# Performance work log

Hardware: AMD Instinct MI355X
Metric: run time of the kernel (lower is better)

The kernel has to match this reference:

```python
import jax, jax.numpy as jnp
import numpy as np

DIM = 64      # d_model, expand=1 -> d_inner = DIM
H_IN = 128
W_IN = 128
DS = 8        # d_state
DTR = 4       # dt_rank = ceil(DIM/16)
DCONV = 4     # conv kernel size
NDIR = 4      # bimamba v6: h-fwd, h-bwd, w-fwd, w-bwd


def layernorm(x, g, b, eps=1e-5):
    m = x.mean(-1, keepdims=True)
    v = x.var(-1, keepdims=True)
    return (x - m) / jnp.sqrt(v + eps) * g + b


def causal_conv(x, w, b):
    # x: (B, L, D), w: (D, 1, K) depthwise, causal left pad
    xt = x.transpose(0, 2, 1)  # (B, D, L)
    y = jax.lax.conv_general_dilated(xt, w, (1,), [(DCONV - 1, 0)],
                                     feature_group_count=xt.shape[1])
    return y.transpose(0, 2, 1) + b


def selective_scan(u, delta, A, Bm, Cm, D):
    # u,delta: (B,L,D); A: (D,N); Bm,Cm: (B,L,N); D: (D,)
    dA = jnp.exp(delta[..., None] * A)                       # (B,L,D,N)
    dBu = delta[..., None] * Bm[:, :, None, :] * u[..., None]

    def comb(c1, c2):
        a1, b1 = c1
        a2, b2 = c2
        return a1 * a2, a2 * b1 + b2

    _, hs = jax.lax.associative_scan(comb, (dA, dBu), axis=1)  # (B,L,D,N)
    return jnp.einsum('bldn,bln->bld', hs, Cm) + u * D


def setup_inputs() -> dict:
    key = jax.random.key(0)
    ks = jax.random.split(key, 12)
    s = 0.02
    inp = {
        'input': jax.random.normal(ks[0], (2, DIM, H_IN, W_IN), jnp.float32),
        'ln_g': jnp.ones((DIM,), jnp.float32),
        'ln_b': jnp.zeros((DIM,), jnp.float32),
        'in_proj_w': jax.random.normal(ks[1], (2 * DIM, DIM), jnp.float32) * s,
        'conv_w': jax.random.normal(ks[2], (NDIR, DIM, 1, DCONV), jnp.float32) * s,
        'conv_b': jnp.zeros((NDIR, DIM), jnp.float32),
        'xproj_w': jax.random.normal(ks[3], (NDIR, DTR + 2 * DS, DIM), jnp.float32) * s,
        'dtproj_w': jax.random.normal(ks[4], (NDIR, DIM, DTR), jnp.float32) * s,
        'dtproj_b': jax.random.normal(ks[5], (NDIR, DIM), jnp.float32) * 0.1,
        'A_log': jnp.broadcast_to(jnp.log(jnp.arange(1.0, DS + 1.0, dtype=jnp.float32)),
                                  (NDIR, DIM, DS)).copy(),
        'D_skip': jnp.ones((NDIR, DIM), jnp.float32),
        'on_g': jnp.ones((DIM,), jnp.float32),
        'on_b': jnp.zeros((DIM,), jnp.float32),
        'out_proj_w': jax.random.normal(ks[6], (DIM, DIM), jnp.float32) * s,
    }
    return inp


def reference(input, ln_g, ln_b, in_proj_w, conv_w, conv_b, xproj_w,
              dtproj_w, dtproj_b, A_log, D_skip, on_g, on_b, out_proj_w):
    B, C, H, W = input.shape
    L = H * W
    seq = input.reshape(B, C, L).transpose(0, 2, 1)           # b (h w) c
    seq = layernorm(seq, ln_g, ln_b)
    xz = seq @ in_proj_w.T                                    # (B,L,2D)
    x, z = jnp.split(xz, 2, axis=-1)

    ar = jnp.arange(L)
    perm = (ar % H) * W + ar // H    # (h w) -> (w h)
    inv = (ar % W) * H + ar // W     # (w h) -> (h w)

    dirs = [(None, False), (None, True), (perm, False), (perm, True)]
    y_sum = jnp.zeros_like(x)
    for i, (p, rev) in enumerate(dirs):
        xd = x if p is None else x[:, p]
        if rev:
            xd = jnp.flip(xd, 1)
        xd = jax.nn.silu(causal_conv(xd, conv_w[i], conv_b[i]))
        dbl = xd @ xproj_w[i].T
        dt, Bm, Cm = jnp.split(dbl, [DTR, DTR + DS], axis=-1)
        dt = jax.nn.softplus(dt @ dtproj_w[i].T + dtproj_b[i])
        A = -jnp.exp(A_log[i])
        yd = selective_scan(xd, dt, A, Bm, Cm, D_skip[i])
        if rev:
            yd = jnp.flip(yd, 1)
        if p is not None:
            yd = yd[:, inv]
        y_sum = y_sum + yd

    y = y_sum / float(NDIR)                 # if_devide_out=True
    y = layernorm(y, on_g, on_b)            # use_norm=True
    y = y * jax.nn.silu(z)                  # gate
    out = y @ out_proj_w.T
    return out.transpose(0, 2, 1).reshape(B, C, H, W) + input
```

## Files before the change

kernel.cpp:

```cpp
#include <hip/hip_runtime.h>
#include <hip/hip_bf16.h>
#include <hip/hip_fp16.h>
#include <cstdint>
#include <cstddef>

#define L_TOT 16384
#define B_SZ 2
#define NROW (B_SZ * L_TOT)
#define CHUNK 32
#define NCH (L_TOT / CHUNK)

static constexpr size_t SLOT_XD  = (size_t)NROW * 64;
static constexpr size_t HSLOT_XD = (size_t)NROW * 64;
static constexpr size_t HSLOT_BC = (size_t)NROW * 16;
static constexpr size_t HSLOT_DT = (size_t)NROW * 64;
static constexpr size_t SLOT_SDT = (size_t)B_SZ * 64 * NCH;
static constexpr size_t SLOT_HC  = (size_t)B_SZ * NCH * 64 * 8;

union H8pack { float4 f4; __half2 h2[4]; };
union H4pack { float2 f2; __half2 h2[2]; };

typedef _Float16 h2v __attribute__((ext_vector_type(2)));
#if __has_builtin(__builtin_amdgcn_fdot2)
#define FDOT2(a, b, c) __builtin_amdgcn_fdot2((a), (b), (c), false)
#else
#define FDOT2(a, b, c) fmaf((float)(a)[0], (float)(b)[0], fmaf((float)(a)[1], (float)(b)[1], (c)))
#endif

__device__ __forceinline__ int tau_map(int dir, int s) {
  int j = (dir & 1) ? (L_TOT - 1 - s) : s;
  if (dir >= 2) j = ((j & 127) << 7) | (j >> 7);
  return j;
}
__device__ __forceinline__ float silu_f(float x) { return x / (1.f + __expf(-x)); }
__device__ __forceinline__ float softplus_f(float x) {
  return fmaxf(x, 0.f) + __logf(1.f + __expf(-fabsf(x)));
}

__global__ void __launch_bounds__(256)
k_ln_inproj(const float* __restrict__ inp, const float* __restrict__ lng,
            const float* __restrict__ lnb, const float* __restrict__ W,
            float* __restrict__ xout, float* __restrict__ zout) {
  __shared__ float xt[64 * 65];
  __shared__ float wrk[8448];
  const int t = threadIdx.x;
  const int lane = t & 63;
  const int w = t >> 6;
  const int b = blockIdx.x >> 8;
  const int l0 = (blockIdx.x & 255) << 6;
  const float* ip = inp + (size_t)b * 64 * L_TOT + l0 + lane;
#pragma unroll 4
  for (int cc = 0; cc < 16; ++cc) {
    int c = cc * 4 + w;
    xt[lane * 65 + c] = ip[(size_t)c * L_TOT];
  }
  __syncthreads();
  {
    float s1 = 0.f, s2 = 0.f;
    const int c0 = w * 16;
#pragma unroll
    for (int cc = 0; cc < 16; ++cc) {
      float v = xt[lane * 65 + c0 + cc];
      s1 += v; s2 = fmaf(v, v, s2);
    }
    wrk[w * 64 + lane] = s1;
    wrk[256 + w * 64 + lane] = s2;
  }
  __syncthreads();
  if (t < 64) {
    float s1 = wrk[t] + wrk[64 + t] + wrk[128 + t] + wrk[192 + t];
    float s2 = wrk[256 + t] + wrk[320 + t] + wrk[384 + t] + wrk[448 + t];
    float m = s1 * 0.015625f;
    float var = s2 * 0.015625f - m * m;
    wrk[512 + t] = m;
    wrk[576 + t] = rsqrtf(var + 1e-5f);
  }
  __syncthreads();
  {
    const float mv = wrk[512 + lane], rv = wrk[576 + lane];
#pragma unroll 4
    for (int k = 0; k < 16; ++k) {
      int c = w + 4 * k;
      float g = lng[c], bb = lnb[c];
      float v = xt[lane * 65 + c];
      xt[lane * 65 + c] = (v - mv) * rv * g + bb;
    }
  }
  __syncthreads();
#pragma unroll 4
  for (int rep = 0; rep < 32; ++rep) {
    int j = rep * 4 + w;
    wrk[j * 65 + lane] = W[(size_t)j * 64 + lane];
  }
  __syncthreads();
  const int rg = lane & 15;
  const int jg = lane >> 4;
  const int j0 = w * 32 + jg * 8;
  const int r0 = rg * 4;
  float acc[4][8] = {};
#pragma unroll 2
  for (int c = 0; c < 64; ++c) {
    float xv[4], wv[8];
#pragma unroll
    for (int i = 0; i < 4; ++i) xv[i] = xt[(r0 + i) * 65 + c];
#pragma unroll
    for (int jj = 0; jj < 8; ++jj) wv[jj] = wrk[(j0 + jj) * 65 + c];
#pragma unroll
    for (int i = 0; i < 4; ++i)
#pragma unroll
      for (int jj = 0; jj < 8; ++jj) acc[i][jj] = fmaf(xv[i], wv[jj], acc[i][jj]);
  }
  __syncthreads();
#pragma unroll
  for (int i = 0; i < 4; ++i)
#pragma unroll
    for (int jj = 0; jj < 8; ++jj) wrk[(r0 + i) * 132 + j0 + jj] = acc[i][jj];
  __syncthreads();
  float* xo = xout + ((size_t)b * L_TOT + l0) * 64;
  float* zo = zout + ((size_t)b * L_TOT + l0) * 64;
#pragma unroll 4
  for (int rep = 0; rep < 16; ++rep) {
    int r = rep * 4 + w;
    xo[(size_t)r * 64 + lane] = wrk[r * 132 + lane];
    zo[(size_t)r * 64 + lane] = wrk[r * 132 + 64 + lane];
  }
}

__global__ void __launch_bounds__(256)
k_convscan(const float* __restrict__ xbuf, const float* __restrict__ cw,
           const float* __restrict__ cb, const float* __restrict__ xpw,
           const float* __restrict__ dtw, const float* __restrict__ dtbias,
           const float* __restrict__ alog,
           __half* __restrict__ xd_base, __half* __restrict__ bc_base,
           __half* __restrict__ dtb_base,
           __half* __restrict__ hcb, __half* __restrict__ sdtb, int dir_base) {
  __shared__ __align__(16) _Float16 xh[67 * 70];
  __shared__ __align__(16) _Float16 wt[20 * 70];
  __shared__ __align__(16) float dbl[64 * 20];
  const int t = threadIdx.x;
  const int lane = t & 63;
  const int w = t >> 6;
  const int slot = blockIdx.y;
  const int dir = dir_base + slot;
  const int blk = blockIdx.x;
  const int b = blk >> 8;
  const int s0 = (blk & 255) << 6;
  const float* xb = xbuf + (size_t)b * L_TOT * 64;
#pragma unroll 1
  for (int i = w; i < 67; i += 4) {
    int s = s0 - 3 + i;
    float v = 0.f;
    if (s >= 0) v = xb[(size_t)tau_map(dir, s) * 64 + lane];
    xh[i * 70 + lane] = (_Float16)v;
  }
#pragma unroll
  for (int jj = 0; jj < 5; ++jj) {
    int j = jj * 4 + w;
    wt[j * 70 + lane] = (_Float16)xpw[((size_t)dir * 20 + j) * 64 + lane];
  }
  __syncthreads();
  float wk[4];
#pragma unroll
  for (int k = 0; k < 4; ++k) wk[k] = cw[(dir * 64 + lane) * 4 + k];
  const float bconv = cb[dir * 64 + lane];
  float u[16];
  __half* xdp = xd_base + (size_t)slot * HSLOT_XD + ((size_t)b * L_TOT + s0) * 64;
#pragma unroll 4
  for (int rr = 0; rr < 16; ++rr) {
    const int r = rr * 4 + w;
    float acc = bconv;
#pragma unroll
    for (int k = 0; k < 4; ++k) acc = fmaf(wk[k], (float)xh[(r + k) * 70 + lane], acc);
    acc = silu_f(acc);
    u[rr] = acc;
    xdp[(size_t)r * 64 + lane] = __float2half(acc);
  }
  __syncthreads();
#pragma unroll 4
  for (int rr = 0; rr < 16; ++rr) xh[(rr * 4 + w) * 70 + lane] = (_Float16)u[rr];
  __syncthreads();
  {
    float acc5[5] = {0.f, 0.f, 0.f, 0.f, 0.f};
    const _Float16* xr = xh + lane * 70;
#pragma unroll 4
    for (int c2 = 0; c2 < 32; ++c2) {
      h2v xv = *(const h2v*)(xr + 2 * c2);
#pragma unroll
      for (int jj = 0; jj < 5; ++jj) {
        h2v wv = *(const h2v*)(wt + (w * 5 + jj) * 70 + 2 * c2);
        acc5[jj] = FDOT2(xv, wv, acc5[jj]);
      }
    }
#pragma unroll
    for (int jj = 0; jj < 5; ++jj) dbl[lane * 20 + w * 5 + jj] = acc5[jj];
  }
  __syncthreads();
  {
    __half* bcp = bc_base + (size_t)slot * HSLOT_BC + ((size_t)b * L_TOT + s0) * 16;
#pragma unroll
    for (int i = t; i < 1024; i += 256) {
      int r = i >> 4, j = i & 15;
      bcp[i] = __float2half(dbl[r * 20 + 4 + j]);
    }
  }
  __half* dtp = dtb_base + (size_t)slot * HSLOT_DT + ((size_t)b * L_TOT + s0) * 64;
  {
    float wdt[4];
#pragma unroll
    for (int r = 0; r < 4; ++r) wdt[r] = dtw[((size_t)dir * 64 + lane) * 4 + r];
    const float bia = dtbias[dir * 64 + lane];
#pragma unroll 4
    for (int rr = 0; rr < 16; ++rr) {
      const int r = rr * 4 + w;
      float dt = bia;
#pragma unroll
      for (int q = 0; q < 4; ++q) dt = fmaf(dbl[r * 20 + q], wdt[q], dt);
      dt = softplus_f(dt);
      dtp[(size_t)r * 64 + lane] = __float2half(dt);
    }
  }
  __syncthreads();
  {
    const int w2 = w & 1;
    const int ng = (w >> 1) << 2;
    const int d = lane;
    const int ch = (s0 >> 5) + w2;
    const float* asrc = alog + ((size_t)dir * 64 + d) * 8;
    float a4[4];
#pragma unroll
    for (int k = 0; k < 4; ++k) a4[k] = -__expf(asrc[ng + k]);
    const float a0 = (ng == 0) ? a4[0] : -__expf(asrc[0]);
    bool pw = true;
#pragma unroll
    for (int k = 0; k < 4; ++k) {
      float tgt = (float)(ng + k + 1) * a0;
      pw = pw && (fabsf(a4[k] - tgt) <= 1e-3f * fabsf(tgt));
    }
    const _Float16* xs = xh + (w2 * 32) * 70;
    const float* ds = dbl + (w2 * 32) * 20;
    const __half* dts = dtp + (size_t)(w2 * 32) * 64;
    float h[4] = {0.f, 0.f, 0.f, 0.f};
    float sdt = 0.f;
    if (pw) {
#pragma unroll 8
      for (int s = 0; s < CHUNK; ++s) {
        float uu = (float)xs[s * 70 + d];
        float dt = __half2float(dts[s * 64 + d]);
        float4 bb = *(const float4*)(ds + s * 20 + 4 + ng);
        sdt += dt;
        float du = dt * uu;
        float p = __expf(dt * a0);
        float p2 = p * p, p4 = p2 * p2;
        float e0, e1, e2, e3;
        if (ng == 0) { e0 = p; e1 = p2; e2 = p2 * p; e3 = p4; }
        else { e0 = p4 * p; e1 = p4 * p2; e2 = e1 * p; e3 = p4 * p4; }
        h[0] = fmaf(e0, h[0], du * bb.x);
        h[1] = fmaf(e1, h[1], du * bb.y);
        h[2] = fmaf(e2, h[2], du * bb.z);
        h[3] = fmaf(e3, h[3], du * bb.w);
      }
    } else {
#pragma unroll 8
      for (int s = 0; s < CHUNK; ++s) {
        float uu = (float)xs[s * 70 + d];
        float dt = __half2float(dts[s * 64 + d]);
        float4 bb = *(const float4*)(ds + s * 20 + 4 + ng);
        sdt += dt;
        float du = dt * uu;
        h[0] = fmaf(__expf(dt * a4[0]), h[0], du * bb.x);
        h[1] = fmaf(__expf(dt * a4[1]), h[1], du * bb.y);
        h[2] = fmaf(__expf(dt * a4[2]), h[2], du * bb.z);
        h[3] = fmaf(__expf(dt * a4[3]), h[3], du * bb.w);
      }
    }
    if (ng == 0)
      sdtb[(size_t)slot * SLOT_SDT + ((size_t)b * 64 + d) * NCH + ch] = __float2half(sdt);
    H4pack pk;
    pk.h2[0] = __floats2half2_rn(h[0], h[1]);
    pk.h2[1] = __floats2half2_rn(h[2], h[3]);
    *(float2*)(hcb + (size_t)slot * SLOT_HC +
               (((size_t)b * NCH + ch) * 64 + d) * 8 + ng) = pk.f2;
  }
}

__global__ void __launch_bounds__(512)
k_scan2(__half* __restrict__ hcb, const __half* __restrict__ sdtb,
        const float* __restrict__ alog, int dir_base) {
  const int t = threadIdx.x;
  const int d = blockIdx.x >> 3;
  const int n = blockIdx.x & 7;
  const int slot = blockIdx.y;
  const int dir = dir_base + slot;
  const int b = blockIdx.z;
  const float a = -__expf(alog[((size_t)dir * 64 + d) * 8 + n]);
  __half* hcp = hcb + (size_t)slot * SLOT_HC + (size_t)b * NCH * 512;
  const __half* sdp = sdtb + (size_t)slot * SLOT_SDT + ((size_t)b * 64 + d) * NCH;
  float e = __expf(a * __half2float(sdp[t]));
  float v = __half2float(hcp[((size_t)t * 64 + d) * 8 + n]);
  __shared__ float sE[NCH], sV[NCH];
  sE[t] = e; sV[t] = v;
  __syncthreads();
#pragma unroll
  for (int off = 1; off < NCH; off <<= 1) {
    float pe = 1.f, pv = 0.f;
    if (t >= off) { pe = sE[t - off]; pv = sV[t - off]; }
    __syncthreads();
    v = fmaf(e, pv, v);
    e = e * pe;
    sE[t] = e; sV[t] = v;
    __syncthreads();
  }
  const float hs = (t == 0) ? 0.f : sV[t - 1];
  hcp[((size_t)t * 64 + d) * 8 + n] = __float2half(hs);
}

__global__ void __launch_bounds__(256, 4)
k_scan3(const __half* __restrict__ xd_in, const __half* __restrict__ bc_base,
        const __half* __restrict__ dtb_base, const __half* __restrict__ hcb,
        const float* __restrict__ alog, const float* __restrict__ dsk,
        float* __restrict__ ysum_f, __half* __restrict__ y_h,
        int dir_base, int scatter) {
  __shared__ __align__(16) float rpl[4 * CHUNK * 16];
  const int t = threadIdx.x;
  const int w = t >> 6;
  const int d = t & 63;
  const int ch = blockIdx.x * 4 + w;
  const int slot = blockIdx.y;
  const int dir = dir_base + slot;
  const int b = blockIdx.z;
  const __half* bcblk = bc_base + (size_t)slot * HSLOT_BC +
                        ((size_t)b * L_TOT + (size_t)blockIdx.x * 4 * CHUNK) * 16;
#pragma unroll
  for (int i = t; i < 4 * CHUNK * 16; i += 256) rpl[i] = __half2float(bcblk[i]);
  __syncthreads();
  const float* rp = rpl + w * CHUNK * 16;
  float a[8];
#pragma unroll
  for (int n = 0; n < 8; ++n) a[n] = -__expf(alog[((size_t)dir * 64 + d) * 8 + n]);
  const float a0 = a[0];
  bool pw = true;
#pragma unroll
  for (int n = 0; n < 8; ++n) {
    float tgt = (float)(n + 1) * a0;
    pw = pw && (fabsf(a[n] - tgt) <= 1e-3f * fabsf(tgt));
  }
  const float Dv = dsk[dir * 64 + d];
  const __half* up  = xd_in + (size_t)slot * HSLOT_XD + ((size_t)b * L_TOT + ch * CHUNK) * 64;
  const __half* dtp = dtb_base + (size_t)slot * HSLOT_DT + ((size_t)b * L_TOT + ch * CHUNK) * 64;
  float h[8];
  {
    H8pack pk;
    pk.f4 = *(const float4*)(hcb + (size_t)slot * SLOT_HC +
                             (((size_t)b * NCH + ch) * 64 + d) * 8);
#pragma unroll
    for (int k = 0; k < 4; ++k) {
      h[2 * k] = __low2float(pk.h2[k]);
      h[2 * k + 1] = __high2float(pk.h2[k]);
    }
  }
  const int sbase = ch * CHUNK;
  if (pw) {
#pragma unroll 8
    for (int s = 0; s < CHUNK; ++s) {
      float u = __half2float(up[s * 64 + d]);
      float dt = __half2float(dtp[s * 64 + d]);
      float4 b0 = *(const float4*)(rp + s * 16);
      float4 b1 = *(const float4*)(rp + s * 16 + 4);
      float4 c0 = *(const float4*)(rp + s * 16 + 8);
      float4 c1 = *(const float4*)(rp + s * 16 + 12);
      float du = dt * u;
      float p = __expf(dt * a0);
      float p2 = p * p, p3 = p2 * p, p4 = p2 * p2;
      float p5 = p4 * p, p6 = p4 * p2, p7 = p4 * p3, p8 = p4 * p4;
      h[0] = fmaf(p,  h[0], du * b0.x);
      h[1] = fmaf(p2, h[1], du * b0.y);
      h[2] = fmaf(p3, h[2], du * b0.z);
      h[3] = fmaf(p4, h[3], du * b0.w);
      h[4] = fmaf(p5, h[4], du * b1.x);
      h[5] = fmaf(p6, h[5], du * b1.y);
      h[6] = fmaf(p7, h[6], du * b1.z);
      h[7] = fmaf(p8, h[7], du * b1.w);
      float y = u * Dv;
      y = fmaf(c0.x, h[0], y); y = fmaf(c0.y, h[1], y);
      y = fmaf(c0.z, h[2], y); y = fmaf(c0.w, h[3], y);
      y = fmaf(c1.x, h[4], y); y = fmaf(c1.y, h[5], y);
      y = fmaf(c1.z, h[6], y); y = fmaf(c1.w, h[7], y);
      if (scatter) {
        int l = tau_map(dir, sbase + s);
        ysum_f[((size_t)b * L_TOT + l) * 64 + d] += y;
      } else {
        y_h[(size_t)slot * HSLOT_XD + ((size_t)b * L_TOT + sbase + s) * 64 + d] = __float2half(y);
      }
    }
  } else {
#pragma unroll 8
    for (int s = 0; s < CHUNK; ++s) {
      float u = __half2float(up[s * 64 + d]);
      float dt = __half2float(dtp[s * 64 + d]);
      float4 b0 = *(const float4*)(rp + s * 16);
      float4 b1 = *(const float4*)(rp + s * 16 + 4);
      float4 c0 = *(const float4*)(rp + s * 16 + 8);
      float4 c1 = *(const float4*)(rp + s * 16 + 12);
      float du = dt * u;
      float y = u * Dv;
      float bv[8] = {b0.x, b0.y, b0.z, b0.w, b1.x, b1.y, b1.z, b1.w};
      float cv[8] = {c0.x, c0.y, c0.z, c0.w, c1.x, c1.y, c1.z, c1.w};
#pragma unroll
      for (int n = 0; n < 8; ++n) {
        h[n] = fmaf(__expf(dt * a[n]), h[n], du * bv[n]);
        y = fmaf(cv[n], h[n], y);
      }
      if (scatter) {
        int l = tau_map(dir, sbase + s);
        ysum_f[((size_t)b * L_TOT + l) * 64 + d] += y;
      } else {
        y_h[(size_t)slot * HSLOT_XD + ((size_t)b * L_TOT + sbase + s) * 64 + d] = __float2half(y);
      }
    }
  }
}

__global__ void __launch_bounds__(256)
k_final(const __half* __restrict__ yh, const float* __restrict__ ysum,
        const float* __restrict__ zbuf,
        const float* __restrict__ ong, const float* __restrict__ onb,
        const float* __restrict__ OW, const float* __restrict__ inp,
        float* __restrict__ out, int gather) {
  __shared__ float xt[64 * 65];
  __shared__ float tzw[64 * 65];
  __shared__ float st[640];
  const int t = threadIdx.x;
  const int lane = t & 63;
  const int w = t >> 6;
  const int b = blockIdx.x >> 8;
  const int l0 = (blockIdx.x & 255) << 6;
#pragma unroll 2
  for (int rep = 0; rep < 16; ++rep) {
    int r = rep * 4 + w;
    int l = l0 + r;
    float acc;
    if (gather) {
      acc = 0.f;
#pragma unroll
      for (int dir = 0; dir < 4; ++dir) {
        int s = tau_map(dir, l);
        acc += __half2float(yh[(size_t)dir * HSLOT_XD + ((size_t)b * L_TOT + s) * 64 + lane]);
      }
    } else {
      acc = ysum[((size_t)b * L_TOT + l) * 64 + lane];
    }
    xt[r * 65 + lane] = acc * 0.25f;
    tzw[r * 65 + lane] = zbuf[((size_t)b * L_TOT + l) * 64 + lane];
  }
  __syncthreads();
  {
    float s1 = 0.f, s2 = 0.f;
    const int c0 = w * 16;
#pragma unroll
    for (int cc = 0; cc < 16; ++cc) {
      float v = xt[lane * 65 + c0 + cc];
      s1 += v; s2 = fmaf(v, v, s2);
    }
    st[w * 64 + lane] = s1;
    st[256 + w * 64 + lane] = s2;
  }
  __syncthreads();
  if (t < 64) {
    float s1 = st[t] + st[64 + t] + st[128 + t] + st[192 + t];
    float s2 = st[256 + t] + st[320 + t] + st[384 + t] + st[448 + t];
    float m = s1 * 0.015625f;
    float var = s2 * 0.015625f - m * m;
    st[512 + t] = m;
    st[576 + t] = rsqrtf(var + 1e-5f);
  }
  __syncthreads();
  {
    const float mv = st[512 + lane], rv = st[576 + lane];
#pragma unroll 4
    for (int k = 0; k < 16; ++k) {
      int c = w + 4 * k;
      float g = ong[c], bb = onb[c];
      float v = xt[lane * 65 + c];
      float zz = tzw[lane * 65 + c];
      xt[lane * 65 + c] = ((v - mv) * rv * g + bb) * silu_f(zz);
    }
  }
  __syncthreads();
#pragma unroll 4
  for (int rep = 0; rep < 16; ++rep) {
    int j = rep * 4 + w;
    tzw[j * 65 + lane] = OW[(size_t)j * 64 + lane];
  }
  __syncthreads();
  const int rg = lane & 15;
  const int jg = lane >> 4;
  const int j0 = w * 16 + jg * 4;
  const int r0 = rg * 4;
  float acc[4][4] = {};
#pragma unroll 2
  for (int c = 0; c < 64; ++c) {
    float xv[4], wv[4];
#pragma unroll
    for (int i = 0; i < 4; ++i) xv[i] = xt[(r0 + i) * 65 + c];
#pragma unroll
    for (int jj = 0; jj < 4; ++jj) wv[jj] = tzw[(j0 + jj) * 65 + c];
#pragma unroll
    for (int i = 0; i < 4; ++i)
#pragma unroll
      for (int jj = 0; jj < 4; ++jj) acc[i][jj] = fmaf(xv[i], wv[jj], acc[i][jj]);
  }
  __syncthreads();
#pragma unroll
  for (int i = 0; i < 4; ++i)
#pragma unroll
    for (int jj = 0; jj < 4; ++jj) xt[(j0 + jj) * 65 + r0 + i] = acc[i][jj];
  __syncthreads();
#pragma unroll 4
  for (int rep = 0; rep < 16; ++rep) {
    int j = rep * 4 + w;
    size_t o = ((size_t)b * 64 + j) * L_TOT + l0 + lane;
    out[o] = xt[j * 65 + lane] + inp[o];
  }
}

extern "C" void kernel_launch(void* const* d_in, const int* in_sizes, int n_in,
                              void* d_out, int out_size, void* d_ws, size_t ws_size,
                              hipStream_t stream) {
  const float* inp    = (const float*)d_in[0];
  const float* lng    = (const float*)d_in[1];
  const float* lnb    = (const float*)d_in[2];
  const float* ipw    = (const float*)d_in[3];
  const float* cw     = (const float*)d_in[4];
  const float* cb     = (const float*)d_in[5];
  const float* xpw    = (const float*)d_in[6];
  const float* dtw    = (const float*)d_in[7];
  const float* dtbias = (const float*)d_in[8];
  const float* alog   = (const float*)d_in[9];
  const float* dsk    = (const float*)d_in[10];
  const float* ong    = (const float*)d_in[11];
  const float* onb    = (const float*)d_in[12];
  const float* opw    = (const float*)d_in[13];
  float* out = (float*)d_out;
  float* ws = (float*)d_ws;

  const size_t half_elems = 4 * (HSLOT_XD + HSLOT_BC + HSLOT_DT + SLOT_SDT + SLOT_HC);
  const size_t need_batched = 2 * SLOT_XD * sizeof(float) + half_elems * sizeof(__half);

  if (ws_size >= need_batched) {
    size_t off = 0;
    float* xbuf = ws + off; off += SLOT_XD;
    float* zbuf = ws + off; off += SLOT_XD;
    __half* hb = (__half*)(ws + off);
    size_t ho = 0;
    __half* xd  = hb + ho; ho += 4 * HSLOT_XD;
    __half* bc  = hb + ho; ho += 4 * HSLOT_BC;
    __half* dtb = hb + ho; ho += 4 * HSLOT_DT;
    __half* sdt = hb + ho; ho += 4 * SLOT_SDT;
    __half* hc  = hb + ho; ho += 4 * SLOT_HC;

    k_ln_inproj<<<dim3(512), 256, 0, stream>>>(inp, lng, lnb, ipw, xbuf, zbuf);
    k_convscan<<<dim3(512, 4), 256, 0, stream>>>(xbuf, cw, cb, xpw, dtw, dtbias, alog,
                                                 xd, bc, dtb, hc, sdt, 0);
    k_scan2<<<dim3(512, 4, B_SZ), NCH, 0, stream>>>(hc, sdt, alog, 0);
    k_scan3<<<dim3(NCH / 4, 4, B_SZ), 256, 0, stream>>>(xd, bc, dtb, hc, alog, dsk,
                                                        nullptr, xd, 0, 0);
    k_final<<<dim3(512), 256, 0, stream>>>(xd, nullptr, zbuf, ong, onb, opw, inp, out, 1);
  } else {
    size_t off = 0;
    float* xbuf = ws + off; off += SLOT_XD;
    float* zbuf = ws + off; off += SLOT_XD;
    float* ysum = ws + off; off += SLOT_XD;
    __half* hb = (__half*)(ws + off);
    size_t ho = 0;
    __half* xd  = hb + ho; ho += HSLOT_XD;
    __half* bc  = hb + ho; ho += HSLOT_BC;
    __half* dtb = hb + ho; ho += HSLOT_DT;
    __half* sdt = hb + ho; ho += SLOT_SDT;
    __half* hc  = hb + ho; ho += SLOT_HC;

    hipMemsetAsync(ysum, 0, SLOT_XD * sizeof(float), stream);
    k_ln_inproj<<<dim3(512), 256, 0, stream>>>(inp, lng, lnb, ipw, xbuf, zbuf);
    for (int d2 = 0; d2 < 4; ++d2) {
      k_convscan<<<dim3(512, 1), 256, 0, stream>>>(xbuf, cw, cb, xpw, dtw, dtbias, alog,
                                                   xd, bc, dtb, hc, sdt, d2);
      k_scan2<<<dim3(512, 1, B_SZ), NCH, 0, stream>>>(hc, sdt, alog, d2);
      k_scan3<<<dim3(NCH / 4, 1, B_SZ), 256, 0, stream>>>(xd, bc, dtb, hc, alog, dsk,
                                                          ysum, nullptr, d2, 1);
    }
    k_final<<<dim3(512), 256, 0, stream>>>(nullptr, ysum, zbuf, ong, onb, opw, inp, out, 0);
  }
}
```

Measured before the change: 125.0 us.

## Store x/z intermediates in fp16 and stage convscan outputs in shared memory

The in-projection now writes x and z as fp16 instead of fp32, which halves the traffic for the intermediate buffers read by the conv/scan and final kernels. In k_convscan, the x_proj results (dbl) and dt are held in shared memory as fp16 with a smaller row pitch. The xd, B/C and dt global stores are deferred to the end of the kernel and issued as contiguous copies, so they no longer interleave with the compute phases. This trades some precision in x, z and the B/C/dt values for lower memory traffic and a smaller shared-memory footprint, which may also raise occupancy.

```diff
diff --git a/kernel.cpp b/kernel.cpp
--- a/kernel.cpp
+++ b/kernel.cpp
@@ -10,7 +10,7 @@
 #define CHUNK 32
 #define NCH (L_TOT / CHUNK)
 
-static constexpr size_t SLOT_XD  = (size_t)NROW * 64;
+static constexpr size_t HSLOT_X  = (size_t)NROW * 64;
 static constexpr size_t HSLOT_XD = (size_t)NROW * 64;
 static constexpr size_t HSLOT_BC = (size_t)NROW * 16;
 static constexpr size_t HSLOT_DT = (size_t)NROW * 64;
@@ -21,6 +21,7 @@
 union H4pack { float2 f2; __half2 h2[2]; };
 
 typedef _Float16 h2v __attribute__((ext_vector_type(2)));
+typedef _Float16 h4v __attribute__((ext_vector_type(4)));
 #if __has_builtin(__builtin_amdgcn_fdot2)
 #define FDOT2(a, b, c) __builtin_amdgcn_fdot2((a), (b), (c), false)
 #else
@@ -40,7 +41,7 @@
 __global__ void __launch_bounds__(256)
 k_ln_inproj(const float* __restrict__ inp, const float* __restrict__ lng,
             const float* __restrict__ lnb, const float* __restrict__ W,
-            float* __restrict__ xout, float* __restrict__ zout) {
+            __half* __restrict__ xout, __half* __restrict__ zout) {
   __shared__ float xt[64 * 65];
   __shared__ float wrk[8448];
   const int t = threadIdx.x;
@@ -116,27 +117,29 @@
 #pragma unroll
     for (int jj = 0; jj < 8; ++jj) wrk[(r0 + i) * 132 + j0 + jj] = acc[i][jj];
   __syncthreads();
-  float* xo = xout + ((size_t)b * L_TOT + l0) * 64;
-  float* zo = zout + ((size_t)b * L_TOT + l0) * 64;
+  __half* xo = xout + ((size_t)b * L_TOT + l0) * 64;
+  __half* zo = zout + ((size_t)b * L_TOT + l0) * 64;
 #pragma unroll 4
   for (int rep = 0; rep < 16; ++rep) {
     int r = rep * 4 + w;
-    xo[(size_t)r * 64 + lane] = wrk[r * 132 + lane];
-    zo[(size_t)r * 64 + lane] = wrk[r * 132 + 64 + lane];
+    xo[(size_t)r * 64 + lane] = __float2half(wrk[r * 132 + lane]);
+    zo[(size_t)r * 64 + lane] = __float2half(wrk[r * 132 + 64 + lane]);
   }
 }
 
 __global__ void __launch_bounds__(256)
-k_convscan(const float* __restrict__ xbuf, const float* __restrict__ cw,
+k_convscan(const __half* __restrict__ xbuf, const float* __restrict__ cw,
            const float* __restrict__ cb, const float* __restrict__ xpw,
            const float* __restrict__ dtw, const float* __restrict__ dtbias,
            const float* __restrict__ alog,
            __half* __restrict__ xd_base, __half* __restrict__ bc_base,
            __half* __restrict__ dtb_base,
            __half* __restrict__ hcb, __half* __restrict__ sdtb, int dir_base) {
-  __shared__ __align__(16) _Float16 xh[67 * 70];
-  __shared__ __align__(16) _Float16 wt[20 * 70];
-  __shared__ __align__(16) float dbl[64 * 20];
+  __shared__ __align__(16) char smem[19968];
+  _Float16* xh  = (_Float16*)smem;
+  _Float16* dbl = (_Float16*)(smem + 8848);
+  _Float16* wt  = (_Float16*)(smem + 11408);
+  _Float16* dts = (_Float16*)(smem + 11408);
   const int t = threadIdx.x;
   const int lane = t & 63;
   const int w = t >> 6;
@@ -145,18 +148,18 @@
   const int blk = blockIdx.x;
   const int b = blk >> 8;
   const int s0 = (blk & 255) << 6;
-  const float* xb = xbuf + (size_t)b * L_TOT * 64;
+  const _Float16* xb = (const _Float16*)xbuf + (size_t)b * L_TOT * 64;
 #pragma unroll 1
   for (int i = w; i < 67; i += 4) {
     int s = s0 - 3 + i;
-    float v = 0.f;
+    _Float16 v = (_Float16)0.f;
     if (s >= 0) v = xb[(size_t)tau_map(dir, s) * 64 + lane];
-    xh[i * 70 + lane] = (_Float16)v;
+    xh[i * 66 + lane] = v;
   }
 #pragma unroll
   for (int jj = 0; jj < 5; ++jj) {
     int j = jj * 4 + w;
-    wt[j * 70 + lane] = (_Float16)xpw[((size_t)dir * 20 + j) * 64 + lane];
+    wt[j * 66 + lane] = (_Float16)xpw[((size_t)dir * 20 + j) * 64 + lane];
   }
   __syncthreads();
   float wk[4];
@@ -164,46 +167,34 @@
   for (int k = 0; k < 4; ++k) wk[k] = cw[(dir * 64 + lane) * 4 + k];
   const float bconv = cb[dir * 64 + lane];
   float u[16];
-  __half* xdp = xd_base + (size_t)slot * HSLOT_XD + ((size_t)b * L_TOT + s0) * 64;
 #pragma unroll 4
   for (int rr = 0; rr < 16; ++rr) {
     const int r = rr * 4 + w;
     float acc = bconv;
 #pragma unroll
-    for (int k = 0; k < 4; ++k) acc = fmaf(wk[k], (float)xh[(r + k) * 70 + lane], acc);
-    acc = silu_f(acc);
-    u[rr] = acc;
-    xdp[(size_t)r * 64 + lane] = __float2half(acc);
-  }
-  __syncthreads();
-#pragma unroll 4
-  for (int rr = 0; rr < 16; ++rr) xh[(rr * 4 + w) * 70 + lane] = (_Float16)u[rr];
+    for (int k = 0; k < 4; ++k) acc = fmaf(wk[k], (float)xh[(r + k) * 66 + lane], acc);
+    u[rr] = silu_f(acc);
+  }
+  __syncthreads();
+#pragma unroll 4
+  for (int rr = 0; rr < 16; ++rr) xh[(rr * 4 + w) * 66 + lane] = (_Float16)u[rr];
   __syncthreads();
   {
     float acc5[5] = {0.f, 0.f, 0.f, 0.f, 0.f};
-    const _Float16* xr = xh + lane * 70;
+    const _Float16* xr = xh + lane * 66;
 #pragma unroll 4
     for (int c2 = 0; c2 < 32; ++c2) {
       h2v xv = *(const h2v*)(xr + 2 * c2);
 #pragma unroll
       for (int jj = 0; jj < 5; ++jj) {
-        h2v wv = *(const h2v*)(wt + (w * 5 + jj) * 70 + 2 * c2);
+        h2v wv = *(const h2v*)(wt + (w * 5 + jj) * 66 + 2 * c2);
         acc5[jj] = FDOT2(xv, wv, acc5[jj]);
       }
     }
 #pragma unroll
-    for (int jj = 0; jj < 5; ++jj) dbl[lane * 20 + w * 5 + jj] = acc5[jj];
-  }
-  __syncthreads();
-  {
-    __half* bcp = bc_base + (size_t)slot * HSLOT_BC + ((size_t)b * L_TOT + s0) * 16;
-#pragma unroll
-    for (int i = t; i < 1024; i += 256) {
-      int r = i >> 4, j = i & 15;
-      bcp[i] = __float2half(dbl[r * 20 + 4 + j]);
-    }
-  }
-  __half* dtp = dtb_base + (size_t)slot * HSLOT_DT + ((size_t)b * L_TOT + s0) * 64;
+    for (int jj = 0; jj < 5; ++jj) dbl[lane * 20 + w * 5 + jj] = (_Float16)acc5[jj];
+  }
+  __syncthreads();
   {
     float wdt[4];
 #pragma unroll
@@ -214,9 +205,8 @@
       const int r = rr * 4 + w;
       float dt = bia;
 #pragma unroll
-      for (int q = 0; q < 4; ++q) dt = fmaf(dbl[r * 20 + q], wdt[q], dt);
-      dt = softplus_f(dt);
-      dtp[(size_t)r * 64 + lane] = __float2half(dt);
+      for (int q = 0; q < 4; ++q) dt = fmaf((float)dbl[r * 20 + q], wdt[q], dt);
+      dts[r * 64 + lane] = (_Float16)softplus_f(dt);
     }
   }
   __syncthreads();
@@ -236,17 +226,17 @@
       float tgt = (float)(ng + k + 1) * a0;
       pw = pw && (fabsf(a4[k] - tgt) <= 1e-3f * fabsf(tgt));
     }
-    const _Float16* xs = xh + (w2 * 32) * 70;
-    const float* ds = dbl + (w2 * 32) * 20;
-    const __half* dts = dtp + (size_t)(w2 * 32) * 64;
+    const _Float16* xs = xh + (w2 * 32) * 66;
+    const _Float16* ds = dbl + (w2 * 32) * 20;
+    const _Float16* dtls = dts + (w2 * 32) * 64;
     float h[4] = {0.f, 0.f, 0.f, 0.f};
     float sdt = 0.f;
     if (pw) {
 #pragma unroll 8
       for (int s = 0; s < CHUNK; ++s) {
-        float uu = (float)xs[s * 70 + d];
-        float dt = __half2float(dts[s * 64 + d]);
-        float4 bb = *(const float4*)(ds + s * 20 + 4 + ng);
+        float uu = (float)xs[s * 66 + d];
+        float dt = (float)dtls[s * 64 + d];
+        h4v bb = *(const h4v*)(ds + s * 20 + 4 + ng);
         sdt += dt;
         float du = dt * uu;
         float p = __expf(dt * a0);
@@ -254,23 +244,23 @@
         float e0, e1, e2, e3;
         if (ng == 0) { e0 = p; e1 = p2; e2 = p2 * p; e3 = p4; }
         else { e0 = p4 * p; e1 = p4 * p2; e2 = e1 * p; e3 = p4 * p4; }
-        h[0] = fmaf(e0, h[0], du * bb.x);
-        h[1] = fmaf(e1, h[1], du * bb.y);
-        h[2] = fmaf(e2, h[2], du * bb.z);
-        h[3] = fmaf(e3, h[3], du * bb.w);
+        h[0] = fmaf(e0, h[0], du * (float)bb[0]);
+        h[1] = fmaf(e1, h[1], du * (float)bb[1]);
+        h[2] = fmaf(e2, h[2], du * (float)bb[2]);
+        h[3] = fmaf(e3, h[3], du * (float)bb[3]);
       }
     } else {
 #pragma unroll 8
       for (int s = 0; s < CHUNK; ++s) {
-        float uu = (float)xs[s * 70 + d];
-        float dt = __half2float(dts[s * 64 + d]);
-        float4 bb = *(const float4*)(ds + s * 20 + 4 + ng);
+        float uu = (float)xs[s * 66 + d];
+        float dt = (float)dtls[s * 64 + d];
+        h4v bb = *(const h4v*)(ds + s * 20 + 4 + ng);
         sdt += dt;
         float du = dt * uu;
-        h[0] = fmaf(__expf(dt * a4[0]), h[0], du * bb.x);
-        h[1] = fmaf(__expf(dt * a4[1]), h[1], du * bb.y);
-        h[2] = fmaf(__expf(dt * a4[2]), h[2], du * bb.z);
-        h[3] = fmaf(__expf(dt * a4[3]), h[3], du * bb.w);
+        h[0] = fmaf(__expf(dt * a4[0]), h[0], du * (float)bb[0]);
+        h[1] = fmaf(__expf(dt * a4[1]), h[1], du * (float)bb[1]);
+        h[2] = fmaf(__expf(dt * a4[2]), h[2], du * (float)bb[2]);
+        h[3] = fmaf(__expf(dt * a4[3]), h[3], du * (float)bb[3]);
       }
     }
     if (ng == 0)
@@ -280,6 +270,24 @@
     pk.h2[1] = __floats2half2_rn(h[2], h[3]);
     *(float2*)(hcb + (size_t)slot * SLOT_HC +
                (((size_t)b * NCH + ch) * 64 + d) * 8 + ng) = pk.f2;
+  }
+  {
+    _Float16* xdp = (_Float16*)xd_base + (size_t)slot * HSLOT_XD +
+                    ((size_t)b * L_TOT + s0) * 64;
+#pragma unroll 4
+    for (int rr = 0; rr < 16; ++rr)
+      xdp[(size_t)(rr * 4 + w) * 64 + lane] = (_Float16)u[rr];
+    _Float16* bcp = (_Float16*)bc_base + (size_t)slot * HSLOT_BC +
+                    ((size_t)b * L_TOT + s0) * 16;
+#pragma unroll
+    for (int i = t; i < 1024; i += 256) {
+      int r = i >> 4, j = i & 15;
+      bcp[i] = dbl[r * 20 + 4 + j];
+    }
+    _Float16* dtp = (_Float16*)dtb_base + (size_t)slot * HSLOT_DT +
+                    ((size_t)b * L_TOT + s0) * 64;
+#pragma unroll
+    for (int i = t; i < 4096; i += 256) dtp[i] = dts[i];
   }
 }
 
@@ -422,7 +430,7 @@
 
 __global__ void __launch_bounds__(256)
 k_final(const __half* __restrict__ yh, const float* __restrict__ ysum,
-        const float* __restrict__ zbuf,
+        const __half* __restrict__ zbuf,
         const float* __restrict__ ong, const float* __restrict__ onb,
         const float* __restrict__ OW, const float* __restrict__ inp,
         float* __restrict__ out, int gather) {
@@ -450,7 +458,7 @@
       acc = ysum[((size_t)b * L_TOT + l) * 64 + lane];
     }
     xt[r * 65 + lane] = acc * 0.25f;
-    tzw[r * 65 + lane] = zbuf[((size_t)b * L_TOT + l) * 64 + lane];
+    tzw[r * 65 + lane] = __half2float(zbuf[((size_t)b * L_TOT + l) * 64 + lane]);
   }
   __syncthreads();
   {
@@ -541,17 +549,16 @@
   const float* onb    = (const float*)d_in[12];
   const float* opw    = (const float*)d_in[13];
   float* out = (float*)d_out;
-  float* ws = (float*)d_ws;
-
-  const size_t half_elems = 4 * (HSLOT_XD + HSLOT_BC + HSLOT_DT + SLOT_SDT + SLOT_HC);
-  const size_t need_batched = 2 * SLOT_XD * sizeof(float) + half_elems * sizeof(__half);
+
+  const size_t half_elems = 2 * HSLOT_X +
+                            4 * (HSLOT_XD + HSLOT_BC + HSLOT_DT + SLOT_SDT + SLOT_HC);
+  const size_t need_batched = half_elems * sizeof(__half);
 
   if (ws_size >= need_batched) {
-    size_t off = 0;
-    float* xbuf = ws + off; off += SLOT_XD;
-    float* zbuf = ws + off; off += SLOT_XD;
-    __half* hb = (__half*)(ws + off);
+    __half* hb = (__half*)d_ws;
     size_t ho = 0;
+    __half* xbuf = hb + ho; ho += HSLOT_X;
+    __half* zbuf = hb + ho; ho += HSLOT_X;
     __half* xd  = hb + ho; ho += 4 * HSLOT_XD;
     __half* bc  = hb + ho; ho += 4 * HSLOT_BC;
     __half* dtb = hb + ho; ho += 4 * HSLOT_DT;
@@ -566,19 +573,20 @@
                                                         nullptr, xd, 0, 0);
     k_final<<<dim3(512), 256, 0, stream>>>(xd, nullptr, zbuf, ong, onb, opw, inp, out, 1);
   } else {
+    float* ws = (float*)d_ws;
     size_t off = 0;
-    float* xbuf = ws + off; off += SLOT_XD;
-    float* zbuf = ws + off; off += SLOT_XD;
-    float* ysum = ws + off; off += SLOT_XD;
+    float* ysum = ws + off; off += (size_t)NROW * 64;
     __half* hb = (__half*)(ws + off);
     size_t ho = 0;
+    __half* xbuf = hb + ho; ho += HSLOT_X;
+    __half* zbuf = hb + ho; ho += HSLOT_X;
     __half* xd  = hb + ho; ho += HSLOT_XD;
     __half* bc  = hb + ho; ho += HSLOT_BC;
     __half* dtb = hb + ho; ho += HSLOT_DT;
     __half* sdt = hb + ho; ho += SLOT_SDT;
     __half* hc  = hb + ho; ho += SLOT_HC;
 
-    hipMemsetAsync(ysum, 0, SLOT_XD * sizeof(float), stream);
+    hipMemsetAsync(ysum, 0, (size_t)NROW * 64 * sizeof(float), stream);
     k_ln_inproj<<<dim3(512), 256, 0, stream>>>(inp, lng, lnb, ipw, xbuf, zbuf);
     for (int d2 = 0; d2 < 4; ++d2) {
       k_convscan<<<dim3(512, 1), 256, 0, stream>>>(xbuf, cw, cb, xpw, dtw, dtbias, alog,
```

Measured after the change: 128.5 us. +2.8%, slower.
